# Kernel optimization log

Measured on AMD Instinct MI355X. Metric: run time of the kernel, lower is better.

## Reference

```python
import jax, jax.numpy as jnp
import numpy as np

INPUT_SIZE = 512
SLOT_SIZE = 256
MLP_HIDDEN = 512
NUM_SLOTS = 8
NUM_ITERS = 3
EPSILON = 1e-6
LN_EPS = 1e-5


def _layernorm(x, g, b):
    m = jnp.mean(x, axis=-1, keepdims=True)
    v = jnp.mean(jnp.square(x - m), axis=-1, keepdims=True)
    return (x - m) * jax.lax.rsqrt(v + LN_EPS) * g + b


def setup_inputs() -> dict:
    key = jax.random.key(0)
    ks = jax.random.split(key, 16)
    N, B, W = 32, 64, 24
    s = 0.02
    inp = {
        "sentence": jax.random.normal(ks[0], (N, B, W, INPUT_SIZE), jnp.float32),
        "sentence_sum": jax.random.normal(ks[1], (N, B, INPUT_SIZE), jnp.float32),
        "mask": jax.random.randint(ks[2], (N, B, W), 0, 2, jnp.int32),
        "Wk": jax.random.normal(ks[3], (INPUT_SIZE, SLOT_SIZE), jnp.float32) * s,
        "bk": jnp.zeros((SLOT_SIZE,), jnp.float32),
        "Wv": jax.random.normal(ks[4], (INPUT_SIZE, SLOT_SIZE), jnp.float32) * s,
        "bv": jnp.zeros((SLOT_SIZE,), jnp.float32),
        "Wq": jax.random.normal(ks[5], (SLOT_SIZE, SLOT_SIZE), jnp.float32) * s,
        "bq": jnp.zeros((SLOT_SIZE,), jnp.float32),
        "g_ln": jnp.ones((SLOT_SIZE,), jnp.float32),
        "b_ln": jnp.zeros((SLOT_SIZE,), jnp.float32),
        "W1": jax.random.normal(ks[6], (SLOT_SIZE, MLP_HIDDEN), jnp.float32) * s,
        "b1": jnp.zeros((MLP_HIDDEN,), jnp.float32),
        "W2": jax.random.normal(ks[7], (MLP_HIDDEN, SLOT_SIZE), jnp.float32) * s,
        "b2": jnp.zeros((SLOT_SIZE,), jnp.float32),
        "Wbind": jax.random.normal(ks[8], (INPUT_SIZE, NUM_SLOTS * SLOT_SIZE), jnp.float32) * s,
        "bbind": jnp.zeros((NUM_SLOTS * SLOT_SIZE,), jnp.float32),
        "Wproj": jax.random.normal(ks[9], (2 * SLOT_SIZE, SLOT_SIZE), jnp.float32) * s,
        "bproj": jnp.zeros((SLOT_SIZE,), jnp.float32),
    }
    return inp


def reference(sentence, sentence_sum, mask, Wk, bk, Wv, bv, Wq, bq, g_ln, b_ln,
              W1, b1, W2, b2, Wbind, bbind, Wproj, bproj):
    N, B = sentence.shape[0], sentence.shape[1]
    # initial slots from the sentence summary: [N, B, NUM_SLOTS, SLOT]
    initial_slots = (sentence_sum @ Wbind + bbind).reshape(N, B, NUM_SLOTS, SLOT_SIZE)
    # additive mask on the word axis: [N, B, W, 1]
    maskf = -1e6 * (1.0 - mask.astype(jnp.float32))[..., None]
    # elu(+1) feature maps for keys; plain linear values
    k = jax.nn.elu(sentence @ Wk + bk) + 1.0  # [N,B,W,SLOT]
    v = sentence @ Wv + bv                    # [N,B,W,SLOT]

    scale = 1.0 / SLOT_SIZE
    slots = initial_slots
    for _ in range(NUM_ITERS):
        q = (slots @ Wq + bq) + initial_slots
        q = jax.nn.elu(q * (SLOT_SIZE ** -0.5)) + 1.0  # [N,B,S,SLOT]
        attn_logits = jnp.einsum('nbis,nbjs->nbij', k, q) + maskf  # [N,B,W,S]
        attn = jax.nn.softmax(attn_logits, axis=3) + EPSILON
        attn = attn / jnp.sum(attn, axis=2, keepdims=True)  # renorm over words
        updates = jnp.einsum('nbij,nbik->nbjk', attn, v)    # [N,B,S,SLOT]
        h = _layernorm(updates, g_ln, b_ln)
        h = jax.nn.relu(h @ W1 + b1) @ W2 + b2
        slots = slots + h * scale

    # dropout is identity in eval mode
    slots = jnp.concatenate([initial_slots, slots], axis=-1)
    slots = slots @ Wproj + bproj
    return slots
```

## Files before the change

### kernel.cpp

```cpp
#include <hip/hip_runtime.h>
#include <hip/hip_bf16.h>
#include <math.h>

typedef unsigned int uint;
typedef unsigned short ushort;
typedef __attribute__((ext_vector_type(8))) short bf16x8;
typedef __attribute__((ext_vector_type(4))) float f32x4;

__device__ __forceinline__ float bu2f(ushort u){ union{uint u; float f;} v; v.u = ((uint)u)<<16; return v.f; }
__device__ __forceinline__ ushort f2bu(float x){ union{float f; uint u;} v; v.f = x; uint r = (v.u + 0x7FFFu + ((v.u>>16)&1u))>>16; return (ushort)r; }
__device__ __forceinline__ uint pack2(float a, float b){ return (uint)f2bu(a) | ((uint)f2bu(b) << 16); }

#define GEPI_IS0  0
#define GEPI_Q    2
#define GEPI_RELU 3
#define GEPI_MLP2 4
#define GEPI_OUT  5

#define SWZ(r, c) (((r) << 5) + ((((c) ^ ((r) >> 1)) & 3) << 3))

template<int EPI>
__global__ __launch_bounds__(256) void gemm64(
    const ushort* __restrict__ Abf, int lda,
    const ushort* __restrict__ Bt,
    const float* __restrict__ xb0,
    float* __restrict__ fp0,
    ushort* __restrict__ up0, ushort* __restrict__ up1,
    int M, int N, int K)
{
    __shared__ ushort As[64 * 32];
    __shared__ ushort Bs[64 * 32];
    int tid = threadIdx.x;
    int wave = tid >> 6, lane = tid & 63;
    int wr = wave >> 1, wc = wave & 1;
    int quad = lane >> 4, l15 = lane & 15;
    int row0 = blockIdx.y * 64, col0 = blockIdx.x * 64;
    int sr = tid >> 2, c4 = tid & 3, sc = c4 * 8;
    int sst = SWZ(sr, c4);

    f32x4 acc[2][2];
    #pragma unroll
    for (int i = 0; i < 2; i++)
        #pragma unroll
        for (int j = 0; j < 2; j++) acc[i][j] = (f32x4){0.f, 0.f, 0.f, 0.f};

    const ushort* Ap = Abf + (size_t)(row0 + sr) * lda + sc;
    const ushort* Bp = Bt  + (size_t)(col0 + sr) * K   + sc;
    uint4 ra = *(const uint4*)Ap;
    uint4 rb = *(const uint4*)Bp;

    for (int k0 = 0; k0 < K; k0 += 32) {
        *(uint4*)&As[sst] = ra;
        *(uint4*)&Bs[sst] = rb;
        __syncthreads();
        if (k0 + 32 < K) {
            ra = *(const uint4*)(Ap + k0 + 32);
            rb = *(const uint4*)(Bp + k0 + 32);
        }
        bf16x8 af[2], bfr[2];
        #pragma unroll
        for (int mt = 0; mt < 2; mt++) {
            int ar = wr * 32 + mt * 16 + l15;
            af[mt] = *(const bf16x8*)&As[SWZ(ar, quad)];
        }
        #pragma unroll
        for (int nt = 0; nt < 2; nt++) {
            int br = wc * 32 + nt * 16 + l15;
            bfr[nt] = *(const bf16x8*)&Bs[SWZ(br, quad)];
        }
        #pragma unroll
        for (int mt = 0; mt < 2; mt++)
            #pragma unroll
            for (int nt = 0; nt < 2; nt++)
                acc[mt][nt] = __builtin_amdgcn_mfma_f32_16x16x32_bf16(
                    af[mt], bfr[nt], acc[mt][nt], 0, 0, 0);
        __syncthreads();
    }

    #pragma unroll
    for (int mt = 0; mt < 2; mt++) {
        #pragma unroll
        for (int nt = 0; nt < 2; nt++) {
            #pragma unroll
            for (int reg = 0; reg < 4; reg++) {
                int gr = row0 + wr * 32 + mt * 16 + quad * 4 + reg;
                int gc = col0 + wc * 32 + nt * 16 + l15;
                float x = acc[mt][nt][reg] + xb0[gc];
                if (EPI == GEPI_IS0) {
                    size_t srow = (size_t)gr * 8 + (gc >> 8);
                    int dim = gc & 255;
                    fp0[srow * 256 + dim] = x;
                    ushort xb = f2bu(x);
                    up0[srow * 512 + dim]       = xb;
                    up0[srow * 512 + 256 + dim] = xb;
                } else if (EPI == GEPI_Q) {
                    float y = (x + bu2f(up1[(size_t)gr * 512 + gc])) * 0.0625f;
                    y = y > 0.f ? y + 1.f : expf(y);
                    up0[(size_t)gr * 256 + gc] = f2bu(y);
                } else if (EPI == GEPI_RELU) {
                    up0[(size_t)gr * 512 + gc] = f2bu(fmaxf(x, 0.f));
                } else if (EPI == GEPI_MLP2) {
                    size_t i = (size_t)gr * 256 + gc;
                    float s = fp0[i] + x * (1.f / 256.f);
                    fp0[i] = s;
                    up0[(size_t)gr * 512 + 256 + gc] = f2bu(s);
                } else {
                    fp0[(size_t)gr * 256 + gc] = x;
                }
            }
        }
    }
}

__global__ __launch_bounds__(256) void gemm_kv64(
    const ushort* __restrict__ A0,
    const ushort* __restrict__ A1,
    const ushort* __restrict__ Bt,
    const float* __restrict__ bk, const float* __restrict__ bv,
    ushort* __restrict__ kbuf, ushort* __restrict__ vbuf, int K)
{
    __shared__ ushort As[64 * 32];
    __shared__ ushort Bs[64 * 32];
    int tid = threadIdx.x;
    int wave = tid >> 6, lane = tid & 63;
    int wr = wave >> 1, wc = wave & 1;
    int quad = lane >> 4, l15 = lane & 15;

    int bid = blockIdx.x;
    int x8  = bid & 7;
    int tt  = bid >> 3;
    int cb  = tt & 7;
    int rb  = (tt >> 3) * 8 + x8;
    int row0 = rb * 64, col0 = cb * 64;
    int sr = tid >> 2, c4 = tid & 3, sc = c4 * 8;
    int sst = SWZ(sr, c4);

    f32x4 acc[2][2];
    #pragma unroll
    for (int i = 0; i < 2; i++)
        #pragma unroll
        for (int j = 0; j < 2; j++) acc[i][j] = (f32x4){0.f, 0.f, 0.f, 0.f};

    const ushort* Ap = (row0 < 32768)
        ? (A0 + (size_t)(row0 + sr) * K + sc)
        : (A1 + (size_t)(row0 - 32768 + sr) * K + sc);
    const ushort* Bp = Bt + (size_t)(col0 + sr) * K + sc;
    uint4 ra = *(const uint4*)Ap;
    uint4 rbv = *(const uint4*)Bp;

    for (int k0 = 0; k0 < K; k0 += 32) {
        *(uint4*)&As[sst] = ra;
        *(uint4*)&Bs[sst] = rbv;
        __syncthreads();
        if (k0 + 32 < K) {
            ra  = *(const uint4*)(Ap + k0 + 32);
            rbv = *(const uint4*)(Bp + k0 + 32);
        }
        bf16x8 af[2], bfr[2];
        #pragma unroll
        for (int mt = 0; mt < 2; mt++) {
            int ar = wr * 32 + mt * 16 + l15;
            af[mt] = *(const bf16x8*)&As[SWZ(ar, quad)];
        }
        #pragma unroll
        for (int nt = 0; nt < 2; nt++) {
            int br = wc * 32 + nt * 16 + l15;
            bfr[nt] = *(const bf16x8*)&Bs[SWZ(br, quad)];
        }
        #pragma unroll
        for (int mt = 0; mt < 2; mt++)
            #pragma unroll
            for (int nt = 0; nt < 2; nt++)
                acc[mt][nt] = __builtin_amdgcn_mfma_f32_16x16x32_bf16(
                    af[mt], bfr[nt], acc[mt][nt], 0, 0, 0);
        __syncthreads();
    }

    bool isK = (col0 < 256);
    const float* __restrict__ bias = isK ? bk : bv;
    ushort* __restrict__ outp = isK ? kbuf : vbuf;
    int cbase = isK ? col0 : col0 - 256;

    #pragma unroll
    for (int mt = 0; mt < 2; mt++) {
        #pragma unroll
        for (int nt = 0; nt < 2; nt++) {
            #pragma unroll
            for (int reg = 0; reg < 4; reg++) {
                int gr = row0 + wr * 32 + mt * 16 + quad * 4 + reg;
                int gc = cbase + wc * 32 + nt * 16 + l15;
                float x = acc[mt][nt][reg] + bias[gc];
                if (isK) x = x > 0.f ? x + 1.f : expf(x);
                outp[(size_t)gr * 256 + gc] = f2bu(x);
            }
        }
    }
}

__global__ __launch_bounds__(256) void prep_kernel(
    const float* __restrict__ sentence,
    const float* __restrict__ sent_sum,
    const float* __restrict__ Wbind, const float* __restrict__ Wk,
    const float* __restrict__ Wv, const float* __restrict__ Wq,
    const float* __restrict__ W1, const float* __restrict__ W2,
    const float* __restrict__ Wproj,
    ushort* __restrict__ sentA0, ushort* __restrict__ sentA1,
    ushort* __restrict__ ssum_bf,
    ushort* __restrict__ Wbind_t, ushort* __restrict__ Wkv_t,
    ushort* __restrict__ Wq_t, ushort* __restrict__ W1_t,
    ushort* __restrict__ W2_t, ushort* __restrict__ Wproj_t)
{
    int gid = blockIdx.x * 256 + threadIdx.x;
    if (gid < 6291456) {
        float4 f = ((const float4*)sentence)[gid];
        uint2 o; o.x = pack2(f.x, f.y); o.y = pack2(f.z, f.w);
        if (gid < 4194304) ((uint2*)sentA0)[gid] = o;
        else               ((uint2*)sentA1)[gid - 4194304] = o;
        return;
    }
    int idx = gid - 6291456;
    if (idx < 262144) {
        float4 f = ((const float4*)sent_sum)[idx];
        uint2 o; o.x = pack2(f.x, f.y); o.y = pack2(f.z, f.w);
        ((uint2*)ssum_bf)[idx] = o; return;
    }
    idx -= 262144;
    if (idx < 1048576) { int n = idx >> 9, k = idx & 511;
        Wbind_t[idx] = f2bu(Wbind[(size_t)k * 2048 + n]); return; }
    idx -= 1048576;
    if (idx < 262144) { int n = idx >> 9, k = idx & 511;
        Wkv_t[idx] = f2bu(n < 256 ? Wk[(size_t)k * 256 + n] : Wv[(size_t)k * 256 + n - 256]); return; }
    idx -= 262144;
    if (idx < 65536) { int n = idx >> 8, k = idx & 255;
        Wq_t[idx] = f2bu(Wq[(size_t)k * 256 + n]); return; }
    idx -= 65536;
    if (idx < 131072) { int n = idx >> 8, k = idx & 255;
        W1_t[idx] = f2bu(W1[(size_t)k * 512 + n]); return; }
    idx -= 131072;
    if (idx < 131072) { int n = idx >> 9, k = idx & 511;
        W2_t[idx] = f2bu(W2[(size_t)k * 256 + n]); return; }
    idx -= 131072;
    if (idx < 131072) { int n = idx >> 9, k = idx & 511;
        Wproj_t[idx] = f2bu(Wproj[(size_t)k * 256 + n]); return; }
}

__global__ __launch_bounds__(256) void attn_kernel(
    const ushort* __restrict__ kbuf, const ushort* __restrict__ vbuf,
    const ushort* __restrict__ qbuf, const int* __restrict__ mask,
    const float* __restrict__ g_ln, const float* __restrict__ b_ln,
    ushort* __restrict__ ubuf)
{
    const int W = 24, S = 8;
    __shared__ ushort kk[24 * 264], vv[24 * 264];
    __shared__ float qs[8 * 257], us[8 * 257];
    __shared__ float attnw[24][8];
    __shared__ float colsum[8], mean_s[8], rstd_s[8], maskf[24];

    int nb = blockIdx.x, t = threadIdx.x;
    size_t bw = (size_t)nb * W * 256, bs = (size_t)nb * S * 256;

    for (int l = t; l < 3072; l += 256) {
        int row = l >> 7, col = l & 127;
        ((uint*)kk)[row * 132 + col] = ((const uint*)(kbuf + bw))[l];
        ((uint*)vv)[row * 132 + col] = ((const uint*)(vbuf + bw))[l];
    }
    for (int l = t; l < 2048; l += 256)
        qs[(l >> 8) * 257 + (l & 255)] = bu2f(qbuf[bs + l]);
    if (t < W) maskf[t] = mask[(size_t)nb * W + t] ? 0.f : -1e6f;
    __syncthreads();

    if (t < W * S) {
        int i = t >> 3, j = t & 7;
        float a = 0.f;
        #pragma unroll 8
        for (int d = 0; d < 256; d++) a += bu2f(kk[i * 264 + d]) * qs[j * 257 + d];
        attnw[i][j] = a + maskf[i];
    }
    __syncthreads();

    if (t < W) {
        float m = attnw[t][0];
        #pragma unroll
        for (int j = 1; j < S; j++) m = fmaxf(m, attnw[t][j]);
        float e[S]; float s = 0.f;
        #pragma unroll
        for (int j = 0; j < S; j++) { e[j] = expf(attnw[t][j] - m); s += e[j]; }
        #pragma unroll
        for (int j = 0; j < S; j++) attnw[t][j] = e[j] / s + 1e-6f;
    }
    __syncthreads();

    if (t < S) {
        float s = 0.f;
        for (int i = 0; i < W; i++) s += attnw[i][t];
        colsum[t] = s;
    }
    __syncthreads();

    {
        float acc[S] = {};
        #pragma unroll
        for (int i = 0; i < W; i++) {
            float vx = bu2f(vv[i * 264 + t]);
            #pragma unroll
            for (int j = 0; j < S; j++) acc[j] += attnw[i][j] * vx;
        }
        #pragma unroll
        for (int j = 0; j < S; j++) us[j * 257 + t] = acc[j] / colsum[j];
    }
    __syncthreads();

    {
        int lane = t & 63;
        #pragma unroll
        for (int jj = 0; jj < 2; jj++) {
            int j = (t >> 6) * 2 + jj;
            float x0 = us[j * 257 + lane],       x1 = us[j * 257 + lane + 64];
            float x2 = us[j * 257 + lane + 128], x3 = us[j * 257 + lane + 192];
            float p = x0 + x1 + x2 + x3;
            for (int off = 32; off; off >>= 1) p += __shfl_xor(p, off);
            float mean = p * (1.f / 256.f);
            float d0 = x0 - mean, d1 = x1 - mean, d2 = x2 - mean, d3 = x3 - mean;
            float vr = d0 * d0 + d1 * d1 + d2 * d2 + d3 * d3;
            for (int off = 32; off; off >>= 1) vr += __shfl_xor(vr, off);
            if (lane == 0) {
                mean_s[j] = mean;
                rstd_s[j] = rsqrtf(vr * (1.f / 256.f) + 1e-5f);
            }
        }
    }
    __syncthreads();

    {
        float g = g_ln[t], bb = b_ln[t];
        #pragma unroll
        for (int j = 0; j < S; j++)
            ubuf[bs + j * 256 + t] = f2bu((us[j * 257 + t] - mean_s[j]) * rstd_s[j] * g + bb);
    }
}

__global__ __launch_bounds__(256) void mega_kernel(
    const float* __restrict__ sentence, const float* __restrict__ sent_sum,
    const int*  __restrict__ mask,
    const float* __restrict__ Wk, const float* __restrict__ bk,
    const float* __restrict__ Wv, const float* __restrict__ bv,
    const float* __restrict__ Wq, const float* __restrict__ bq,
    const float* __restrict__ g_ln, const float* __restrict__ b_ln,
    const float* __restrict__ W1, const float* __restrict__ b1,
    const float* __restrict__ W2, const float* __restrict__ b2,
    const float* __restrict__ Wbind, const float* __restrict__ bbind,
    const float* __restrict__ Wproj, const float* __restrict__ bproj,
    float* __restrict__ out)
{
    const int W = 24, S = 8, D = 256, IN = 512, H = 512;
    __shared__ float seh[2048];
    __shared__ ushort kk[24 * 256];
    __shared__ ushort vv[24 * 256];
    __shared__ float is0s[8 * 256];
    __shared__ float sl[8 * 256];
    __shared__ float qv[8 * 256];
    __shared__ float attnw[24][8];
    __shared__ float colsum[8], mean_s[8], rstd_s[8], maskf[24];

    int nb = blockIdx.x, t = threadIdx.x;
    size_t sbase = (size_t)nb * W * IN;

    if (t < W) maskf[t] = mask[(size_t)nb * W + t] ? 0.f : -1e6f;
    for (int l = t; l < IN; l += 256) seh[l] = sent_sum[(size_t)nb * IN + l];
    __syncthreads();
    {
        float acc[S];
        #pragma unroll
        for (int j = 0; j < S; j++) acc[j] = bbind[j * D + t];
        for (int c = 0; c < IN; c++) {
            float sc = seh[c];
            #pragma unroll
            for (int j = 0; j < S; j++) acc[j] += sc * Wbind[(size_t)c * (S * D) + j * D + t];
        }
        #pragma unroll
        for (int j = 0; j < S; j++) { is0s[j * D + t] = acc[j]; sl[j * D + t] = acc[j]; }
    }
    {
        float ka[W], va[W];
        float bkv = bk[t], bvv = bv[t];
        #pragma unroll
        for (int i = 0; i < W; i++) { ka[i] = bkv; va[i] = bvv; }
        for (int ch = 0; ch < 8; ch++) {
            __syncthreads();
            for (int l = t; l < W * 64; l += 256) {
                int i = l >> 6, c = l & 63;
                seh[l] = sentence[sbase + (size_t)i * IN + ch * 64 + c];
            }
            __syncthreads();
            for (int c = 0; c < 64; c++) {
                int cg = ch * 64 + c;
                float wk = Wk[(size_t)cg * D + t];
                float wv = Wv[(size_t)cg * D + t];
                #pragma unroll
                for (int i = 0; i < W; i++) {
                    float s = seh[i * 64 + c];
                    ka[i] += s * wk; va[i] += s * wv;
                }
            }
        }
        #pragma unroll
        for (int i = 0; i < W; i++) {
            float kx = ka[i];
            kk[i * D + t] = f2bu(kx > 0.f ? kx + 1.f : expf(kx));
            vv[i * D + t] = f2bu(va[i]);
        }
    }
    __syncthreads();

    for (int it = 0; it < 3; it++) {
        {
            float qa[S]; float bqv = bq[t];
            #pragma unroll
            for (int j = 0; j < S; j++) qa[j] = bqv + is0s[j * D + t];
            for (int c = 0; c < D; c++) {
                float wq = Wq[(size_t)c * D + t];
                #pragma unroll
                for (int j = 0; j < S; j++) qa[j] += sl[j * D + c] * wq;
            }
            #pragma unroll
            for (int j = 0; j < S; j++) {
                float y = qa[j] * 0.0625f;
                qv[j * D + t] = y > 0.f ? y + 1.f : expf(y);
            }
        }
        __syncthreads();
        if (t < W * S) {
            int i = t >> 3, j = t & 7;
            float a = 0.f;
            #pragma unroll 8
            for (int d = 0; d < D; d++) a += bu2f(kk[i * D + d]) * qv[j * D + d];
            attnw[i][j] = a + maskf[i];
        }
        __syncthreads();
        if (t < W) {
            float m = attnw[t][0];
            #pragma unroll
            for (int j = 1; j < S; j++) m = fmaxf(m, attnw[t][j]);
            float e[S]; float s = 0.f;
            #pragma unroll
            for (int j = 0; j < S; j++) { e[j] = expf(attnw[t][j] - m); s += e[j]; }
            #pragma unroll
            for (int j = 0; j < S; j++) attnw[t][j] = e[j] / s + 1e-6f;
        }
        __syncthreads();
        if (t < S) {
            float s = 0.f;
            for (int i = 0; i < W; i++) s += attnw[i][t];
            colsum[t] = s;
        }
        __syncthreads();
        {
            float acc[S] = {};
            #pragma unroll
            for (int i = 0; i < W; i++) {
                float vx = bu2f(vv[i * D + t]);
                #pragma unroll
                for (int j = 0; j < S; j++) acc[j] += attnw[i][j] * vx;
            }
            #pragma unroll
            for (int j = 0; j < S; j++) qv[j * D + t] = acc[j] / colsum[j];
        }
        __syncthreads();
        {
            int lane = t & 63;
            #pragma unroll
            for (int jj = 0; jj < 2; jj++) {
                int j = (t >> 6) * 2 + jj;
                float x0 = qv[j * D + lane],       x1 = qv[j * D + lane + 64];
                float x2 = qv[j * D + lane + 128], x3 = qv[j * D + lane + 192];
                float p = x0 + x1 + x2 + x3;
                for (int off = 32; off; off >>= 1) p += __shfl_xor(p, off);
                float mean = p * (1.f / 256.f);
                float d0 = x0 - mean, d1 = x1 - mean, d2 = x2 - mean, d3 = x3 - mean;
                float vr = d0 * d0 + d1 * d1 + d2 * d2 + d3 * d3;
                for (int off = 32; off; off >>= 1) vr += __shfl_xor(vr, off);
                if (lane == 0) { mean_s[j] = mean; rstd_s[j] = rsqrtf(vr * (1.f / 256.f) + 1e-5f); }
            }
        }
        __syncthreads();
        {
            float g = g_ln[t], bb = b_ln[t];
            #pragma unroll
            for (int j = 0; j < S; j++)
                qv[j * D + t] = (qv[j * D + t] - mean_s[j]) * rstd_s[j] * g + bb;
        }
        __syncthreads();
        {
            float sa[S]; float b2v = b2[t];
            #pragma unroll
            for (int j = 0; j < S; j++) sa[j] = b2v;
            for (int half = 0; half < 2; half++) {
                int hcol = half * 256 + t;
                float ha[S]; float b1v = b1[hcol];
                #pragma unroll
                for (int j = 0; j < S; j++) ha[j] = b1v;
                for (int d = 0; d < D; d++) {
                    float w1 = W1[(size_t)d * H + hcol];
                    #pragma unroll
                    for (int j = 0; j < S; j++) ha[j] += qv[j * D + d] * w1;
                }
                __syncthreads();
                #pragma unroll
                for (int j = 0; j < S; j++) seh[j * D + t] = fmaxf(ha[j], 0.f);
                __syncthreads();
                for (int h = 0; h < 256; h++) {
                    float w2 = W2[(size_t)(half * 256 + h) * D + t];
                    #pragma unroll
                    for (int j = 0; j < S; j++) sa[j] += seh[j * D + h] * w2;
                }
            }
            __syncthreads();
            #pragma unroll
            for (int j = 0; j < S; j++) sl[j * D + t] += sa[j] * (1.f / 256.f);
        }
        __syncthreads();
    }
    {
        float oa[S]; float bpv = bproj[t];
        #pragma unroll
        for (int j = 0; j < S; j++) oa[j] = bpv;
        for (int c = 0; c < D; c++) {
            float wp1 = Wproj[(size_t)c * D + t];
            float wp2 = Wproj[(size_t)(D + c) * D + t];
            #pragma unroll
            for (int j = 0; j < S; j++)
                oa[j] += is0s[j * D + c] * wp1 + sl[j * D + c] * wp2;
        }
        #pragma unroll
        for (int j = 0; j < S; j++)
            out[(size_t)nb * (S * D) + j * D + t] = oa[j];
    }
}

extern "C" void kernel_launch(void* const* d_in, const int* in_sizes, int n_in,
                              void* d_out, int out_size, void* d_ws, size_t ws_size,
                              hipStream_t stream)
{
    const float* sentence = (const float*)d_in[0];
    const float* sent_sum = (const float*)d_in[1];
    const int*  mask      = (const int*)d_in[2];
    const float* Wk = (const float*)d_in[3];  const float* bk = (const float*)d_in[4];
    const float* Wv = (const float*)d_in[5];  const float* bv = (const float*)d_in[6];
    const float* Wq = (const float*)d_in[7];  const float* bq = (const float*)d_in[8];
    const float* g_ln = (const float*)d_in[9];  const float* b_ln = (const float*)d_in[10];
    const float* W1 = (const float*)d_in[11]; const float* b1 = (const float*)d_in[12];
    const float* W2 = (const float*)d_in[13]; const float* b2 = (const float*)d_in[14];
    const float* Wbind = (const float*)d_in[15]; const float* bbind = (const float*)d_in[16];
    const float* Wproj = (const float*)d_in[17]; const float* bproj = (const float*)d_in[18];
    float* out = (float*)d_out;

    const size_t WS_NEEDED = 123076608ULL;
    if (ws_size >= WS_NEEDED) {
        char* w = (char*)d_ws;
        float*  slots   = (float*) (w);
        ushort* catb    = (ushort*)(w + 16777216);
        ushort* kbuf    = (ushort*)(w + 33554432);
        ushort* vbuf    = (ushort*)(w + 58720256);
        ushort* qbuf    = (ushort*)(w + 83886080);
        ushort* ubuf    = (ushort*)(w + 92274688);
        ushort* hbuf    = (ushort*)(w + 100663296);
        ushort* ssum_bf = (ushort*)(w + 117440512);
        ushort* Wbind_t = (ushort*)(w + 119537664);
        ushort* Wkv_t   = (ushort*)(w + 121634816);
        ushort* Wq_t    = (ushort*)(w + 122159104);
        ushort* W1_t    = (ushort*)(w + 122290176);
        ushort* W2_t    = (ushort*)(w + 122552320);
        ushort* Wproj_t = (ushort*)(w + 122814464);

        ushort* sentA0 = (ushort*)(w);
        ushort* sentA1 = (ushort*)(w + 83886080);

        prep_kernel<<<dim3(32512), dim3(256), 0, stream>>>(
            sentence, sent_sum, Wbind, Wk, Wv, Wq, W1, W2, Wproj,
            sentA0, sentA1,
            ssum_bf, Wbind_t, Wkv_t, Wq_t, W1_t, W2_t, Wproj_t);

        gemm_kv64<<<dim3(6144), dim3(256), 0, stream>>>(
            sentA0, sentA1, Wkv_t, bk, bv, kbuf, vbuf, 512);

        gemm64<GEPI_IS0><<<dim3(32, 32), dim3(256), 0, stream>>>(
            ssum_bf, 512, Wbind_t, bbind,
            slots, catb, nullptr, 2048, 2048, 512);

        for (int it = 0; it < 3; it++) {
            gemm64<GEPI_Q><<<dim3(4, 256), dim3(256), 0, stream>>>(
                catb + 256, 512, Wq_t, bq,
                nullptr, qbuf, catb, 16384, 256, 256);
            attn_kernel<<<dim3(2048), dim3(256), 0, stream>>>(
                kbuf, vbuf, qbuf, mask, g_ln, b_ln, ubuf);
            gemm64<GEPI_RELU><<<dim3(8, 256), dim3(256), 0, stream>>>(
                ubuf, 256, W1_t, b1,
                nullptr, hbuf, nullptr, 16384, 512, 256);
            gemm64<GEPI_MLP2><<<dim3(4, 256), dim3(256), 0, stream>>>(
                hbuf, 512, W2_t, b2,
                slots, catb, nullptr, 16384, 256, 512);
        }

        gemm64<GEPI_OUT><<<dim3(4, 256), dim3(256), 0, stream>>>(
            catb, 512, Wproj_t, bproj,
            out, nullptr, nullptr, 16384, 256, 512);
    } else {
        mega_kernel<<<dim3(2048), dim3(256), 0, stream>>>(
            sentence, sent_sum, mask, Wk, bk, Wv, bv, Wq, bq, g_ln, b_ln,
            W1, b1, W2, b2, Wbind, bbind, Wproj, bproj, out);
    }
}
```

Baseline: 520.9 us.

## Fuse sentence fp32-to-bf16 conversion into KV GEMM and enlarge tiles to 128x128

```diff
diff --git a/kernel.cpp b/kernel.cpp
--- a/kernel.cpp
+++ b/kernel.cpp
@@ -112,15 +112,14 @@
     }
 }
 
-__global__ __launch_bounds__(256) void gemm_kv64(
-    const ushort* __restrict__ A0,
-    const ushort* __restrict__ A1,
+__global__ __launch_bounds__(256) void gemm_kv128(
+    const float* __restrict__ A,
     const ushort* __restrict__ Bt,
     const float* __restrict__ bk, const float* __restrict__ bv,
     ushort* __restrict__ kbuf, ushort* __restrict__ vbuf, int K)
 {
-    __shared__ ushort As[64 * 32];
-    __shared__ ushort Bs[64 * 32];
+    __shared__ ushort As[128 * 32];
+    __shared__ ushort Bs[128 * 32];
     int tid = threadIdx.x;
     int wave = tid >> 6, lane = tid & 63;
     int wr = wave >> 1, wc = wave & 1;
@@ -129,48 +128,59 @@
     int bid = blockIdx.x;
     int x8  = bid & 7;
     int tt  = bid >> 3;
-    int cb  = tt & 7;
-    int rb  = (tt >> 3) * 8 + x8;
-    int row0 = rb * 64, col0 = cb * 64;
+    int cb  = tt & 3;
+    int rb  = (tt >> 2) * 8 + x8;
+    int row0 = rb * 128, col0 = cb * 128;
+
     int sr = tid >> 2, c4 = tid & 3, sc = c4 * 8;
-    int sst = SWZ(sr, c4);
-
-    f32x4 acc[2][2];
+    int sst0 = SWZ(sr, c4), sst1 = SWZ(sr + 64, c4);
+
+    f32x4 acc[4][4];
     #pragma unroll
-    for (int i = 0; i < 2; i++)
-        #pragma unroll
-        for (int j = 0; j < 2; j++) acc[i][j] = (f32x4){0.f, 0.f, 0.f, 0.f};
-
-    const ushort* Ap = (row0 < 32768)
-        ? (A0 + (size_t)(row0 + sr) * K + sc)
-        : (A1 + (size_t)(row0 - 32768 + sr) * K + sc);
-    const ushort* Bp = Bt + (size_t)(col0 + sr) * K + sc;
-    uint4 ra = *(const uint4*)Ap;
-    uint4 rbv = *(const uint4*)Bp;
+    for (int i = 0; i < 4; i++)
+        #pragma unroll
+        for (int j = 0; j < 4; j++) acc[i][j] = (f32x4){0.f, 0.f, 0.f, 0.f};
+
+    const float*  Ap0 = A  + (size_t)(row0 + sr) * K + sc;
+    const float*  Ap1 = A  + (size_t)(row0 + 64 + sr) * K + sc;
+    const ushort* Bp0 = Bt + (size_t)(col0 + sr) * K + sc;
+    const ushort* Bp1 = Bt + (size_t)(col0 + 64 + sr) * K + sc;
+
+    float4 a00 = *(const float4*)Ap0, a01 = *(const float4*)(Ap0 + 4);
+    float4 a10 = *(const float4*)Ap1, a11 = *(const float4*)(Ap1 + 4);
+    uint4  b0  = *(const uint4*)Bp0,  b1  = *(const uint4*)Bp1;
 
     for (int k0 = 0; k0 < K; k0 += 32) {
-        *(uint4*)&As[sst] = ra;
-        *(uint4*)&Bs[sst] = rbv;
+        uint4 ua0, ua1;
+        ua0.x = pack2(a00.x, a00.y); ua0.y = pack2(a00.z, a00.w);
+        ua0.z = pack2(a01.x, a01.y); ua0.w = pack2(a01.z, a01.w);
+        ua1.x = pack2(a10.x, a10.y); ua1.y = pack2(a10.z, a10.w);
+        ua1.z = pack2(a11.x, a11.y); ua1.w = pack2(a11.z, a11.w);
+        *(uint4*)&As[sst0] = ua0;
+        *(uint4*)&As[sst1] = ua1;
+        *(uint4*)&Bs[sst0] = b0;
+        *(uint4*)&Bs[sst1] = b1;
         __syncthreads();
         if (k0 + 32 < K) {
-            ra  = *(const uint4*)(Ap + k0 + 32);
-            rbv = *(const uint4*)(Bp + k0 + 32);
-        }
-        bf16x8 af[2], bfr[2];
-        #pragma unroll
-        for (int mt = 0; mt < 2; mt++) {
-            int ar = wr * 32 + mt * 16 + l15;
+            a00 = *(const float4*)(Ap0 + k0 + 32); a01 = *(const float4*)(Ap0 + k0 + 36);
+            a10 = *(const float4*)(Ap1 + k0 + 32); a11 = *(const float4*)(Ap1 + k0 + 36);
+            b0  = *(const uint4*)(Bp0 + k0 + 32);  b1  = *(const uint4*)(Bp1 + k0 + 32);
+        }
+        bf16x8 af[4], bfr[4];
+        #pragma unroll
+        for (int mt = 0; mt < 4; mt++) {
+            int ar = wr * 64 + mt * 16 + l15;
             af[mt] = *(const bf16x8*)&As[SWZ(ar, quad)];
         }
         #pragma unroll
-        for (int nt = 0; nt < 2; nt++) {
-            int br = wc * 32 + nt * 16 + l15;
+        for (int nt = 0; nt < 4; nt++) {
+            int br = wc * 64 + nt * 16 + l15;
             bfr[nt] = *(const bf16x8*)&Bs[SWZ(br, quad)];
         }
         #pragma unroll
-        for (int mt = 0; mt < 2; mt++)
-            #pragma unroll
-            for (int nt = 0; nt < 2; nt++)
+        for (int mt = 0; mt < 4; mt++)
+            #pragma unroll
+            for (int nt = 0; nt < 4; nt++)
                 acc[mt][nt] = __builtin_amdgcn_mfma_f32_16x16x32_bf16(
                     af[mt], bfr[nt], acc[mt][nt], 0, 0, 0);
         __syncthreads();
@@ -182,13 +192,13 @@
     int cbase = isK ? col0 : col0 - 256;
 
     #pragma unroll
-    for (int mt = 0; mt < 2; mt++) {
-        #pragma unroll
-        for (int nt = 0; nt < 2; nt++) {
+    for (int mt = 0; mt < 4; mt++) {
+        #pragma unroll
+        for (int nt = 0; nt < 4; nt++) {
             #pragma unroll
             for (int reg = 0; reg < 4; reg++) {
-                int gr = row0 + wr * 32 + mt * 16 + quad * 4 + reg;
-                int gc = cbase + wc * 32 + nt * 16 + l15;
+                int gr = row0 + wr * 64 + mt * 16 + quad * 4 + reg;
+                int gc = cbase + wc * 64 + nt * 16 + l15;
                 float x = acc[mt][nt][reg] + bias[gc];
                 if (isK) x = x > 0.f ? x + 1.f : expf(x);
                 outp[(size_t)gr * 256 + gc] = f2bu(x);
@@ -198,33 +208,23 @@
 }
 
 __global__ __launch_bounds__(256) void prep_kernel(
-    const float* __restrict__ sentence,
     const float* __restrict__ sent_sum,
     const float* __restrict__ Wbind, const float* __restrict__ Wk,
     const float* __restrict__ Wv, const float* __restrict__ Wq,
     const float* __restrict__ W1, const float* __restrict__ W2,
     const float* __restrict__ Wproj,
-    ushort* __restrict__ sentA0, ushort* __restrict__ sentA1,
     ushort* __restrict__ ssum_bf,
     ushort* __restrict__ Wbind_t, ushort* __restrict__ Wkv_t,
     ushort* __restrict__ Wq_t, ushort* __restrict__ W1_t,
     ushort* __restrict__ W2_t, ushort* __restrict__ Wproj_t)
 {
     int gid = blockIdx.x * 256 + threadIdx.x;
-    if (gid < 6291456) {
-        float4 f = ((const float4*)sentence)[gid];
+    if (gid < 262144) {
+        float4 f = ((const float4*)sent_sum)[gid];
         uint2 o; o.x = pack2(f.x, f.y); o.y = pack2(f.z, f.w);
-        if (gid < 4194304) ((uint2*)sentA0)[gid] = o;
-        else               ((uint2*)sentA1)[gid - 4194304] = o;
-        return;
-    }
-    int idx = gid - 6291456;
-    if (idx < 262144) {
-        float4 f = ((const float4*)sent_sum)[idx];
-        uint2 o; o.x = pack2(f.x, f.y); o.y = pack2(f.z, f.w);
-        ((uint2*)ssum_bf)[idx] = o; return;
-    }
-    idx -= 262144;
+        ((uint2*)ssum_bf)[gid] = o; return;
+    }
+    int idx = gid - 262144;
     if (idx < 1048576) { int n = idx >> 9, k = idx & 511;
         Wbind_t[idx] = f2bu(Wbind[(size_t)k * 2048 + n]); return; }
     idx -= 1048576;
@@ -572,16 +572,12 @@
         ushort* W2_t    = (ushort*)(w + 122552320);
         ushort* Wproj_t = (ushort*)(w + 122814464);
 
-        ushort* sentA0 = (ushort*)(w);
-        ushort* sentA1 = (ushort*)(w + 83886080);
-
-        prep_kernel<<<dim3(32512), dim3(256), 0, stream>>>(
-            sentence, sent_sum, Wbind, Wk, Wv, Wq, W1, W2, Wproj,
-            sentA0, sentA1,
+        prep_kernel<<<dim3(7936), dim3(256), 0, stream>>>(
+            sent_sum, Wbind, Wk, Wv, Wq, W1, W2, Wproj,
             ssum_bf, Wbind_t, Wkv_t, Wq_t, W1_t, W2_t, Wproj_t);
 
-        gemm_kv64<<<dim3(6144), dim3(256), 0, stream>>>(
-            sentA0, sentA1, Wkv_t, bk, bv, kbuf, vbuf, 512);
+        gemm_kv128<<<dim3(1536), dim3(256), 0, stream>>>(
+            sentence, Wkv_t, bk, bv, kbuf, vbuf, 512);
 
         gemm64<GEPI_IS0><<<dim3(32, 32), dim3(256), 0, stream>>>(
             ssum_bf, 512, Wbind_t, bbind,
```

New measurement: 516.7 us. About the same (-0.8%).

## Fuse sentence bf16 conversion into KV GEMM loads and vectorise attention LDS reads

Applied to the files above, without the earlier changes.

```diff
diff --git a/kernel.cpp b/kernel.cpp
--- a/kernel.cpp
+++ b/kernel.cpp
@@ -112,9 +112,8 @@
     }
 }
 
-__global__ __launch_bounds__(256) void gemm_kv64(
-    const ushort* __restrict__ A0,
-    const ushort* __restrict__ A1,
+__global__ __launch_bounds__(256) void gemm_kv64f(
+    const float* __restrict__ A,
     const ushort* __restrict__ Bt,
     const float* __restrict__ bk, const float* __restrict__ bv,
     ushort* __restrict__ kbuf, ushort* __restrict__ vbuf, int K)
@@ -141,19 +140,21 @@
         #pragma unroll
         for (int j = 0; j < 2; j++) acc[i][j] = (f32x4){0.f, 0.f, 0.f, 0.f};
 
-    const ushort* Ap = (row0 < 32768)
-        ? (A0 + (size_t)(row0 + sr) * K + sc)
-        : (A1 + (size_t)(row0 - 32768 + sr) * K + sc);
+    const float*  Ap = A  + (size_t)(row0 + sr) * K + sc;
     const ushort* Bp = Bt + (size_t)(col0 + sr) * K + sc;
-    uint4 ra = *(const uint4*)Ap;
-    uint4 rbv = *(const uint4*)Bp;
+    float4 ra0 = *(const float4*)Ap, ra1 = *(const float4*)(Ap + 4);
+    uint4  rbv = *(const uint4*)Bp;
 
     for (int k0 = 0; k0 < K; k0 += 32) {
-        *(uint4*)&As[sst] = ra;
+        uint4 ua;
+        ua.x = pack2(ra0.x, ra0.y); ua.y = pack2(ra0.z, ra0.w);
+        ua.z = pack2(ra1.x, ra1.y); ua.w = pack2(ra1.z, ra1.w);
+        *(uint4*)&As[sst] = ua;
         *(uint4*)&Bs[sst] = rbv;
         __syncthreads();
         if (k0 + 32 < K) {
-            ra  = *(const uint4*)(Ap + k0 + 32);
+            ra0 = *(const float4*)(Ap + k0 + 32);
+            ra1 = *(const float4*)(Ap + k0 + 36);
             rbv = *(const uint4*)(Bp + k0 + 32);
         }
         bf16x8 af[2], bfr[2];
@@ -198,33 +199,23 @@
 }
 
 __global__ __launch_bounds__(256) void prep_kernel(
-    const float* __restrict__ sentence,
     const float* __restrict__ sent_sum,
     const float* __restrict__ Wbind, const float* __restrict__ Wk,
     const float* __restrict__ Wv, const float* __restrict__ Wq,
     const float* __restrict__ W1, const float* __restrict__ W2,
     const float* __restrict__ Wproj,
-    ushort* __restrict__ sentA0, ushort* __restrict__ sentA1,
     ushort* __restrict__ ssum_bf,
     ushort* __restrict__ Wbind_t, ushort* __restrict__ Wkv_t,
     ushort* __restrict__ Wq_t, ushort* __restrict__ W1_t,
     ushort* __restrict__ W2_t, ushort* __restrict__ Wproj_t)
 {
     int gid = blockIdx.x * 256 + threadIdx.x;
-    if (gid < 6291456) {
-        float4 f = ((const float4*)sentence)[gid];
+    if (gid < 262144) {
+        float4 f = ((const float4*)sent_sum)[gid];
         uint2 o; o.x = pack2(f.x, f.y); o.y = pack2(f.z, f.w);
-        if (gid < 4194304) ((uint2*)sentA0)[gid] = o;
-        else               ((uint2*)sentA1)[gid - 4194304] = o;
-        return;
-    }
-    int idx = gid - 6291456;
-    if (idx < 262144) {
-        float4 f = ((const float4*)sent_sum)[idx];
-        uint2 o; o.x = pack2(f.x, f.y); o.y = pack2(f.z, f.w);
-        ((uint2*)ssum_bf)[idx] = o; return;
-    }
-    idx -= 262144;
+        ((uint2*)ssum_bf)[gid] = o; return;
+    }
+    int idx = gid - 262144;
     if (idx < 1048576) { int n = idx >> 9, k = idx & 511;
         Wbind_t[idx] = f2bu(Wbind[(size_t)k * 2048 + n]); return; }
     idx -= 1048576;
@@ -251,8 +242,8 @@
     ushort* __restrict__ ubuf)
 {
     const int W = 24, S = 8;
-    __shared__ ushort kk[24 * 264], vv[24 * 264];
-    __shared__ float qs[8 * 257], us[8 * 257];
+    __shared__ ushort kk[24 * 264], vv[24 * 264], qsb[8 * 264];
+    __shared__ float us[8 * 257];
     __shared__ float attnw[24][8];
     __shared__ float colsum[8], mean_s[8], rstd_s[8], maskf[24];
 
@@ -264,16 +255,23 @@
         ((uint*)kk)[row * 132 + col] = ((const uint*)(kbuf + bw))[l];
         ((uint*)vv)[row * 132 + col] = ((const uint*)(vbuf + bw))[l];
     }
-    for (int l = t; l < 2048; l += 256)
-        qs[(l >> 8) * 257 + (l & 255)] = bu2f(qbuf[bs + l]);
+    for (int l = t; l < 1024; l += 256) {
+        int row = l >> 7, col = l & 127;
+        ((uint*)qsb)[row * 132 + col] = ((const uint*)(qbuf + bs))[l];
+    }
     if (t < W) maskf[t] = mask[(size_t)nb * W + t] ? 0.f : -1e6f;
     __syncthreads();
 
     if (t < W * S) {
         int i = t >> 3, j = t & 7;
         float a = 0.f;
-        #pragma unroll 8
-        for (int d = 0; d < 256; d++) a += bu2f(kk[i * 264 + d]) * qs[j * 257 + d];
+        for (int d0 = 0; d0 < 256; d0 += 8) {
+            bf16x8 kv8 = *(const bf16x8*)&kk[i * 264 + d0];
+            bf16x8 qv8 = *(const bf16x8*)&qsb[j * 264 + d0];
+            #pragma unroll
+            for (int m = 0; m < 8; m++)
+                a += bu2f((ushort)kv8[m]) * bu2f((ushort)qv8[m]);
+        }
         attnw[i][j] = a + maskf[i];
     }
     __syncthreads();
@@ -302,8 +300,12 @@
         #pragma unroll
         for (int i = 0; i < W; i++) {
             float vx = bu2f(vv[i * 264 + t]);
-            #pragma unroll
-            for (int j = 0; j < S; j++) acc[j] += attnw[i][j] * vx;
+            float4 w0 = *(const float4*)&attnw[i][0];
+            float4 w1 = *(const float4*)&attnw[i][4];
+            acc[0] += w0.x * vx; acc[1] += w0.y * vx;
+            acc[2] += w0.z * vx; acc[3] += w0.w * vx;
+            acc[4] += w1.x * vx; acc[5] += w1.y * vx;
+            acc[6] += w1.z * vx; acc[7] += w1.w * vx;
         }
         #pragma unroll
         for (int j = 0; j < S; j++) us[j * 257 + t] = acc[j] / colsum[j];
@@ -572,16 +574,12 @@
         ushort* W2_t    = (ushort*)(w + 122552320);
         ushort* Wproj_t = (ushort*)(w + 122814464);
 
-        ushort* sentA0 = (ushort*)(w);
-        ushort* sentA1 = (ushort*)(w + 83886080);
-
-        prep_kernel<<<dim3(32512), dim3(256), 0, stream>>>(
-            sentence, sent_sum, Wbind, Wk, Wv, Wq, W1, W2, Wproj,
-            sentA0, sentA1,
+        prep_kernel<<<dim3(7936), dim3(256), 0, stream>>>(
+            sent_sum, Wbind, Wk, Wv, Wq, W1, W2, Wproj,
             ssum_bf, Wbind_t, Wkv_t, Wq_t, W1_t, W2_t, Wproj_t);
 
-        gemm_kv64<<<dim3(6144), dim3(256), 0, stream>>>(
-            sentA0, sentA1, Wkv_t, bk, bv, kbuf, vbuf, 512);
+        gemm_kv64f<<<dim3(6144), dim3(256), 0, stream>>>(
+            sentence, Wkv_t, bk, bv, kbuf, vbuf, 512);
 
         gemm64<GEPI_IS0><<<dim3(32, 32), dim3(256), 0, stream>>>(
             ssum_bf, 512, Wbind_t, bbind,
```

After: 510.1 us. 1.02x faster.
